# Kernel tuning notes

Hardware: AMD Instinct MI355X
Metric: run time of the kernel (lower is better)

Reference implementation:

```python
import jax, jax.numpy as jnp
import numpy as np

N = 500_000
K = 16
E = N * K
H = 256


def _linear_params(key, fan_in, fan_out):
    k1, k2 = jax.random.split(key)
    bound = 1.0 / np.sqrt(fan_in)
    W = jax.random.uniform(k1, (fan_in, fan_out), jnp.float32, -bound, bound)
    b = jax.random.uniform(k2, (fan_out,), jnp.float32, -bound, bound)
    return W, b


def setup_inputs() -> dict:
    key = jax.random.key(0)
    ks = jax.random.split(key, 10)
    x = jax.random.normal(ks[0], (N, 3), jnp.float32)
    edge_index = jax.random.randint(ks[1], (2, E), 0, N, jnp.int64)
    edge_attr = jax.random.normal(ks[2], (E, 1), jnp.float32)
    W1, b1 = _linear_params(ks[3], K, H)          # GNN1 message MLP: Linear(k, 256)
    We1, be1 = _linear_params(ks[4], H, 128)      # encoder Linear(256,128)
    We2, be2 = _linear_params(ks[5], 128, 6)      # encoder Linear(128,6)
    Wd1, bd1 = _linear_params(ks[6], 6, 128)      # decoder Linear(6,128)
    Wd2, bd2 = _linear_params(ks[7], 128, H)      # decoder Linear(128,256)
    Wo, bo = _linear_params(ks[8], H, 1)          # output Linear(256,1)
    return {"x": x, "edge_index": edge_index, "edge_attr": edge_attr,
            "W1": W1, "b1": b1, "We1": We1, "be1": be1, "We2": We2, "be2": be2,
            "Wd1": Wd1, "bd1": bd1, "Wd2": Wd2, "bd2": bd2, "Wo": Wo, "bo": bo}


def reference(x, edge_index, edge_attr, W1, b1, We1, be1, We2, be2,
              Wd1, bd1, Wd2, bd2, Wo, bo):
    # GNN1: messages are edge_attr verbatim (x_i/x_j ignored); aggregate reshapes
    # all E scalar messages into (N, k) (k edges per node, contiguous) and runs
    # Linear(k,256)+Tanh. Note: LSTM and GCN4 branches in the torch code are dead
    # (GNN1 ignores its node-feature input), so they do not affect the output.
    k = W1.shape[0]
    msgs = edge_attr.reshape(-1, k)                    # (N, k)
    h = jnp.tanh(msgs @ W1 + b1)                       # (N, 256)
    # second L1 call produces the identical result (depends only on edge_attr)
    z = jnp.tanh(jnp.tanh(h @ We1 + be1) @ We2 + be2)  # encoder -> (N, 6)
    d = jnp.tanh(z @ Wd1 + bd1) @ Wd2 + bd2            # decoder -> (N, 256)
    out = jax.nn.sigmoid(jnp.tanh(d) @ Wo + bo)        # (N, 1)
    return out[:, 0]                                   # squeeze(dim=1) -> (N,)
```

## Files before the change

### kernel.cpp

```cpp
#include <hip/hip_runtime.h>


#define N_NODES 500000

#define OFF_W1 0
#define OFF_W2 8192
#define OFF_W3 73728
#define OFF_W4 77824
#define OFF_W5 86016
#define OFF_WO 151552
#define OFF_B1 152576
#define OFF_B2 153600
#define OFF_B3 154112
#define OFF_B4 154176
#define OFF_B5 154688
#define OFF_EXTRA 155712
#define OFF_ZERO  155728
#define IMG_END   156240
#define IMG_ALLOC 156672

#define K1_B1    77824
#define K1_B2    78848
#define K1_B3    79360
#define K1_Z     79872
#define K1_LDS   80384
#define K2_LDS   76800
#define K2_W4    0
#define K2_W5    8192
#define K2_WO    73728
#define K2_B4    74752
#define K2_B5    75264

#define SCONST (-2.8853900817779268f)

typedef _Float16 half8  __attribute__((ext_vector_type(8)));
typedef __fp16   pk16x2 __attribute__((ext_vector_type(2)));
typedef float    f32x4  __attribute__((ext_vector_type(4)));
typedef int      int4v  __attribute__((ext_vector_type(4)));

__device__ __align__(16) char g_img[IMG_ALLOC];

static __device__ __forceinline__ unsigned pack_f16_rne(float a, float b) {
  _Float16 ha = (_Float16)a, hb = (_Float16)b;
  unsigned short ua = __builtin_bit_cast(unsigned short, ha);
  unsigned short ub = __builtin_bit_cast(unsigned short, hb);
  return (unsigned)ua | ((unsigned)ub << 16);
}
static __device__ __forceinline__ int pkrtz(float a, float b) {
  pk16x2 h = __builtin_amdgcn_cvt_pkrtz(a, b);
  return __builtin_bit_cast(int, h);
}
static __device__ __forceinline__ float sig2(float y) {
  float e = __builtin_amdgcn_exp2f(y);
  return __builtin_amdgcn_rcpf(1.0f + e);
}
static __device__ __forceinline__ float sigmoid_f(float x) {
  float e = __builtin_amdgcn_exp2f(x * -1.4426950408889634f);
  return __builtin_amdgcn_rcpf(1.0f + e);
}
static __device__ __forceinline__ f32x4 mfma16(half8 a, int4v b, f32x4 c) {
  return __builtin_amdgcn_mfma_f32_16x16x32_f16(a, __builtin_bit_cast(half8, b), c, 0, 0, 0);
}
static __device__ __forceinline__ half8 lda(const char* smem, int off) {
  return *(const half8*)(smem + off);
}
static __device__ __forceinline__ f32x4 ldf4(const char* smem, int off) {
  return *(const f32x4*)(smem + off);
}
#define FENCE() __builtin_amdgcn_sched_barrier(0)

struct PK2 { int lo, hi; };
static __device__ __forceinline__ PK2 tp(f32x4 a) {
  PK2 p;
  p.lo = pkrtz(sig2(a.x), sig2(a.y));
  p.hi = pkrtz(sig2(a.z), sig2(a.w));
  return p;
}

__global__ void gnn_prep(const float* __restrict__ W1,  const float* __restrict__ b1,
                         const float* __restrict__ We1, const float* __restrict__ be1,
                         const float* __restrict__ We2, const float* __restrict__ be2,
                         const float* __restrict__ Wd1, const float* __restrict__ bd1,
                         const float* __restrict__ Wd2, const float* __restrict__ bd2,
                         const float* __restrict__ Wo,  const float* __restrict__ bo)
{
  int t = blockIdx.x * 256 + threadIdx.x;
  int off = t * 4;
  if (off >= IMG_END) return;
  unsigned val;
  if (off < OFF_W2) {
    int rel = off;
    int mi = rel >> 9, li = (rel >> 4) & 31, j2 = (rel >> 2) & 3;
    int fout = mi * 16 + (li & 15);
    int k0 = (li >> 4) * 8 + j2 * 2;
    val = pack_f16_rne(SCONST * W1[k0 * 256 + fout], SCONST * W1[(k0 + 1) * 256 + fout]);
  } else if (off < OFF_W3) {
    int rel = off - OFF_W2;
    int blk = rel >> 10, li = (rel >> 4) & 63, j2 = (rel >> 2) & 3;
    int mi = blk >> 3, ki = blk & 7;
    int fout = mi * 16 + (li & 15);
    int k0 = ki * 32 + 4 * (li >> 4) + 16 * (j2 >> 1) + 2 * (j2 & 1);
    val = pack_f16_rne(2.0f * SCONST * We1[k0 * 128 + fout],
                       2.0f * SCONST * We1[(k0 + 1) * 128 + fout]);
  } else if (off < OFF_W4) {
    int rel = off - OFF_W3;
    int ki = rel >> 10, li = (rel >> 4) & 63, j2 = (rel >> 2) & 3;
    int fo = li & 15;
    int k0 = ki * 32 + 4 * (li >> 4) + 16 * (j2 >> 1) + 2 * (j2 & 1);
    float a = (fo < 6) ? 2.0f * SCONST * We2[k0 * 6 + fo] : 0.0f;
    float b = (fo < 6) ? 2.0f * SCONST * We2[(k0 + 1) * 6 + fo] : 0.0f;
    val = pack_f16_rne(a, b);
  } else if (off < OFF_W5) {
    int rel = off - OFF_W4;
    int mi = rel >> 10, li = (rel >> 4) & 63, j2 = (rel >> 2) & 3;
    int fout = mi * 16 + (li & 15);
    int qa = li >> 4;
    unsigned v = 0;
    if (j2 < 2) {
      int k0 = 4 * qa + 2 * j2;
      float a = (k0 < 6)     ? 2.0f * SCONST * Wd1[k0 * 128 + fout]       : 0.0f;
      float b = (k0 + 1 < 6) ? 2.0f * SCONST * Wd1[(k0 + 1) * 128 + fout] : 0.0f;
      v = pack_f16_rne(a, b);
    }
    val = v;
  } else if (off < OFF_WO) {
    int rel = off - OFF_W5;
    int blk = rel >> 10, li = (rel >> 4) & 63, j2 = (rel >> 2) & 3;
    int mi = blk >> 2, ki = blk & 3;
    int fout = mi * 16 + (li & 15);
    int k0 = ki * 32 + 4 * (li >> 4) + 16 * (j2 >> 1) + 2 * (j2 & 1);
    val = pack_f16_rne(2.0f * SCONST * Wd2[k0 * 256 + fout],
                       2.0f * SCONST * Wd2[(k0 + 1) * 256 + fout]);
  } else if (off < OFF_B1) {
    val = __builtin_bit_cast(unsigned, 2.0f * Wo[(off - OFF_WO) >> 2]);
  } else if (off < OFF_B2) {
    val = __builtin_bit_cast(unsigned, SCONST * b1[(off - OFF_B1) >> 2]);
  } else if (off < OFF_B3) {
    int i = (off - OFF_B2) >> 2;
    float s = 0.0f;
    for (int k = 0; k < 256; ++k) s += We1[k * 128 + i];
    val = __builtin_bit_cast(unsigned, SCONST * (be1[i] - s));
  } else if (off < OFF_B4) {
    int i = (off - OFF_B3) >> 2;
    float v = 0.0f;
    if (i < 6) {
      float s = 0.0f;
      for (int k = 0; k < 128; ++k) s += We2[k * 6 + i];
      v = SCONST * (be2[i] - s);
    }
    val = __builtin_bit_cast(unsigned, v);
  } else if (off < OFF_B5) {
    int i = (off - OFF_B4) >> 2;
    float s = 0.0f;
    for (int k = 0; k < 6; ++k) s += Wd1[k * 128 + i];
    val = __builtin_bit_cast(unsigned, SCONST * (bd1[i] - s));
  } else if (off < OFF_EXTRA) {
    int i = (off - OFF_B5) >> 2;
    float s = 0.0f;
    for (int k = 0; k < 128; ++k) s += Wd2[k * 256 + i];
    val = __builtin_bit_cast(unsigned, SCONST * (bd2[i] - s));
  } else if (off == OFF_EXTRA) {
    float s = 0.0f;
    for (int k = 0; k < 256; ++k) s += Wo[k];
    val = __builtin_bit_cast(unsigned, bo[0] - s);
  } else {
    val = 0;
  }
  *(unsigned*)(g_img + off) = val;
}

static __device__ __forceinline__ void stage_chunk(const char* src, char* dst) {
  __builtin_amdgcn_global_load_lds(
      (const __attribute__((address_space(1))) void*)src,
      (__attribute__((address_space(3))) void*)dst, 16, 0, 0);
}

#define L1_PAIR(KO, OUT_G0, OUT_G1) do {                                   \
    half8 Ae = lda(smem, w1b + (2*(KO))*w1s);                              \
    half8 Ao = lda(smem, w1b + (2*(KO)+1)*w1s);                            \
    f32x4 be_ = ldf4(smem, K1_B1 + (2*(KO))*64 + q*16);                    \
    f32x4 bo_ = ldf4(smem, K1_B1 + (2*(KO)+1)*64 + q*16);                  \
    f32x4 ae0 = mfma16(Ae, b1g0, be_);                                     \
    f32x4 ae1 = mfma16(Ae, b1g1, be_);                                     \
    f32x4 ao0 = mfma16(Ao, b1g0, bo_);                                     \
    f32x4 ao1 = mfma16(Ao, b1g1, bo_);                                     \
    PK2 pe0 = tp(ae0), po0 = tp(ao0), pe1 = tp(ae1), po1 = tp(ao1);        \
    OUT_G0.x = pe0.lo; OUT_G0.y = pe0.hi; OUT_G0.z = po0.lo; OUT_G0.w = po0.hi; \
    OUT_G1.x = pe1.lo; OUT_G1.y = pe1.hi; OUT_G1.z = po1.lo; OUT_G1.w = po1.hi; \
    FENCE();                                                               \
  } while (0)

#define L2_MI(MI, ACC0, ACC1) do {                                                            \
    f32x4 bb = ldf4(smem, K1_B2 + (MI)*64 + q*16);                                            \
    ACC0 = bb; ACC1 = bb;                                                                     \
    half8 A;                                                                                  \
    A = lda(smem, OFF_W2 + ((MI)*8+0)*1024 + ln*16); ACC0 = mfma16(A, c2g0_0, ACC0); ACC1 = mfma16(A, c2g1_0, ACC1); \
    A = lda(smem, OFF_W2 + ((MI)*8+1)*1024 + ln*16); ACC0 = mfma16(A, c2g0_1, ACC0); ACC1 = mfma16(A, c2g1_1, ACC1); \
    A = lda(smem, OFF_W2 + ((MI)*8+2)*1024 + ln*16); ACC0 = mfma16(A, c2g0_2, ACC0); ACC1 = mfma16(A, c2g1_2, ACC1); \
    A = lda(smem, OFF_W2 + ((MI)*8+3)*1024 + ln*16); ACC0 = mfma16(A, c2g0_3, ACC0); ACC1 = mfma16(A, c2g1_3, ACC1); \
    A = lda(smem, OFF_W2 + ((MI)*8+4)*1024 + ln*16); ACC0 = mfma16(A, c2g0_4, ACC0); ACC1 = mfma16(A, c2g1_4, ACC1); \
    A = lda(smem, OFF_W2 + ((MI)*8+5)*1024 + ln*16); ACC0 = mfma16(A, c2g0_5, ACC0); ACC1 = mfma16(A, c2g1_5, ACC1); \
    A = lda(smem, OFF_W2 + ((MI)*8+6)*1024 + ln*16); ACC0 = mfma16(A, c2g0_6, ACC0); ACC1 = mfma16(A, c2g1_6, ACC1); \
    A = lda(smem, OFF_W2 + ((MI)*8+7)*1024 + ln*16); ACC0 = mfma16(A, c2g0_7, ACC0); ACC1 = mfma16(A, c2g1_7, ACC1); \
  } while (0)

#define L2_PAIR(KO, OUT_G0, OUT_G1) do {                                   \
    f32x4 ve0, ve1, vo0, vo1;                                              \
    L2_MI(2*(KO),   ve0, ve1);                                             \
    FENCE();                                                               \
    L2_MI(2*(KO)+1, vo0, vo1);                                             \
    PK2 pe0 = tp(ve0), po0 = tp(vo0), pe1 = tp(ve1), po1 = tp(vo1);        \
    OUT_G0.x = pe0.lo; OUT_G0.y = pe0.hi; OUT_G0.z = po0.lo; OUT_G0.w = po0.hi; \
    OUT_G1.x = pe1.lo; OUT_G1.y = pe1.hi; OUT_G1.z = po1.lo; OUT_G1.w = po1.hi; \
    FENCE();                                                               \
  } while (0)

__global__ __launch_bounds__(512)
void gnn_k1(const float* __restrict__ ea, int4v* __restrict__ zbuf)
{
  __shared__ __align__(16) char smem[K1_LDS];
  const int tid = threadIdx.x;
  const int wv = tid >> 6, ln = tid & 63;

#pragma unroll 1
  for (int r = 0; r < 10; ++r) {
    int cb = (r * 8 + wv) << 6;
    if (cb < 5024) {
      int src;
      if (cb < 4864)      src = cb * 16;
      else if (cb < 4992) src = OFF_B1 + (cb - 4864) * 16;
      else                src = OFF_ZERO + (cb - 4992) * 16;
      stage_chunk(g_img + src + ln * 16, smem + (size_t)cb * 16 + ln * 16);
    }
  }
  __syncthreads();

  const int q = ln >> 4, c = ln & 15;
  const bool qlo = (q < 2);
  const int lnl16 = (ln & 31) * 16;
  const int w1b = qlo ? (OFF_W1 + lnl16) : (K1_Z + lnl16);
  const int w1s = qlo ? 512 : 0;

  const int NT = (N_NODES + 255) / 256;
#pragma unroll 1
  for (int t = blockIdx.x; t < NT; t += gridDim.x) {
    const int base = t * 256 + wv * 32;

    int nl = base + (q >> 1) * 16 + c;
    if (nl > N_NODES - 1) nl = N_NODES - 1;
    const f32x4* ea4 = (const f32x4*)ea;
    size_t eb = (size_t)nl * 4 + (size_t)((q & 1) * 2);
    f32x4 vlo = ea4[eb];
    f32x4 vhi = ea4[eb + 1];
    int4v b1g0;
    b1g0.x = pkrtz(vlo.x, vlo.y); b1g0.y = pkrtz(vlo.z, vlo.w);
    b1g0.z = pkrtz(vhi.x, vhi.y); b1g0.w = pkrtz(vhi.z, vhi.w);
    int sh = (ln + 32) & 63;
    int4v b1g1;
    b1g1.x = __shfl(b1g0.x, sh, 64); b1g1.y = __shfl(b1g0.y, sh, 64);
    b1g1.z = __shfl(b1g0.z, sh, 64); b1g1.w = __shfl(b1g0.w, sh, 64);

    int4v c2g0_0, c2g0_1, c2g0_2, c2g0_3, c2g0_4, c2g0_5, c2g0_6, c2g0_7;
    int4v c2g1_0, c2g1_1, c2g1_2, c2g1_3, c2g1_4, c2g1_5, c2g1_6, c2g1_7;
    L1_PAIR(0, c2g0_0, c2g1_0);
    L1_PAIR(1, c2g0_1, c2g1_1);
    L1_PAIR(2, c2g0_2, c2g1_2);
    L1_PAIR(3, c2g0_3, c2g1_3);
    L1_PAIR(4, c2g0_4, c2g1_4);
    L1_PAIR(5, c2g0_5, c2g1_5);
    L1_PAIR(6, c2g0_6, c2g1_6);
    L1_PAIR(7, c2g0_7, c2g1_7);

    int4v c3g0_0, c3g0_1, c3g0_2, c3g0_3;
    int4v c3g1_0, c3g1_1, c3g1_2, c3g1_3;
    L2_PAIR(0, c3g0_0, c3g1_0);
    L2_PAIR(1, c3g0_1, c3g1_1);
    L2_PAIR(2, c3g0_2, c3g1_2);
    L2_PAIR(3, c3g0_3, c3g1_3);

    f32x4 bb3 = ldf4(smem, K1_B3 + q * 16);
    f32x4 z0 = bb3, z1 = bb3;
    half8 A;
    A = lda(smem, OFF_W3 + 0 * 1024 + ln * 16); z0 = mfma16(A, c3g0_0, z0); z1 = mfma16(A, c3g1_0, z1);
    A = lda(smem, OFF_W3 + 1 * 1024 + ln * 16); z0 = mfma16(A, c3g0_1, z0); z1 = mfma16(A, c3g1_1, z1);
    A = lda(smem, OFF_W3 + 2 * 1024 + ln * 16); z0 = mfma16(A, c3g0_2, z0); z1 = mfma16(A, c3g1_2, z1);
    A = lda(smem, OFF_W3 + 3 * 1024 + ln * 16); z0 = mfma16(A, c3g0_3, z0); z1 = mfma16(A, c3g1_3, z1);
    PK2 p3g0 = tp(z0);
    PK2 p3g1 = tp(z1);

    if (ln < 32) {
      int4v zv;
      zv.x = p3g0.lo; zv.y = p3g0.hi; zv.z = p3g1.lo; zv.w = p3g1.hi;
      zbuf[(size_t)(t * 8 + wv) * 32 + ln] = zv;
    }
  }
}

#define L4_MI(MI, ACC0, ACC1) do {                                         \
    f32x4 bb = ldf4(smem, K2_B4 + (MI)*64 + q*16);                         \
    half8 A = lda(smem, K2_W4 + (MI)*1024 + ln*16);                        \
    ACC0 = mfma16(A, b4g0, bb);                                            \
    ACC1 = mfma16(A, b4g1, bb);                                            \
  } while (0)

#define L4_PAIR(KO, OUT_G0, OUT_G1) do {                                   \
    f32x4 ve0, ve1, vo0, vo1;                                              \
    L4_MI(2*(KO),   ve0, ve1);                                             \
    L4_MI(2*(KO)+1, vo0, vo1);                                             \
    PK2 pe0 = tp(ve0), po0 = tp(vo0), pe1 = tp(ve1), po1 = tp(vo1);        \
    OUT_G0.x = pe0.lo; OUT_G0.y = pe0.hi; OUT_G0.z = po0.lo; OUT_G0.w = po0.hi; \
    OUT_G1.x = pe1.lo; OUT_G1.y = pe1.hi; OUT_G1.z = po1.lo; OUT_G1.w = po1.hi; \
    FENCE();                                                               \
  } while (0)

#define L5_MI(MI) do {                                                                        \
    f32x4 bb = ldf4(smem, K2_B5 + (MI)*64 + q*16);                                            \
    f32x4 a0 = bb, a1 = bb;                                                                   \
    half8 A;                                                                                  \
    A = lda(smem, K2_W5 + ((MI)*4+0)*1024 + ln*16); a0 = mfma16(A, c5g0_0, a0); a1 = mfma16(A, c5g1_0, a1); \
    A = lda(smem, K2_W5 + ((MI)*4+1)*1024 + ln*16); a0 = mfma16(A, c5g0_1, a0); a1 = mfma16(A, c5g1_1, a1); \
    A = lda(smem, K2_W5 + ((MI)*4+2)*1024 + ln*16); a0 = mfma16(A, c5g0_2, a0); a1 = mfma16(A, c5g1_2, a1); \
    A = lda(smem, K2_W5 + ((MI)*4+3)*1024 + ln*16); a0 = mfma16(A, c5g0_3, a0); a1 = mfma16(A, c5g1_3, a1); \
    f32x4 wo = ldf4(smem, K2_WO + (MI)*64 + q*16);                                            \
    part0 += sig2(a0.x)*wo.x + sig2(a0.y)*wo.y + sig2(a0.z)*wo.z + sig2(a0.w)*wo.w;           \
    part1 += sig2(a1.x)*wo.x + sig2(a1.y)*wo.y + sig2(a1.z)*wo.z + sig2(a1.w)*wo.w;           \
    FENCE();                                                                                  \
  } while (0)

__global__ __launch_bounds__(512)
void gnn_k2(const int4v* __restrict__ zbuf, float* __restrict__ out)
{
  __shared__ __align__(16) char smem[K2_LDS];
  const int tid = threadIdx.x;
  const int wv = tid >> 6, ln = tid & 63;

#pragma unroll 1
  for (int r = 0; r < 10; ++r) {
    int cb = (r * 8 + wv) << 6;
    if (cb < 4800) {
      int src;
      if (cb < 512)       src = OFF_W4 + cb * 16;
      else if (cb < 4672) src = OFF_W5 + (cb - 512) * 16;
      else                src = OFF_B4 + (cb - 4672) * 16;
      stage_chunk(g_img + src + ln * 16, smem + (size_t)cb * 16 + ln * 16);
    }
  }
  __syncthreads();

  const int q = ln >> 4, c = ln & 15;
  const float bo2 = *(const float*)(g_img + OFF_EXTRA);

  const int NT = (N_NODES + 255) / 256;
#pragma unroll 1
  for (int t = blockIdx.x; t < NT; t += gridDim.x) {
    const int base = t * 256 + wv * 32;

    int4v zv = {0, 0, 0, 0};
    if (ln < 32) zv = zbuf[(size_t)(t * 8 + wv) * 32 + ln];

    int4v b4g0, b4g1;
    b4g0.x = zv.x; b4g0.y = zv.y; b4g0.z = 0; b4g0.w = 0;
    b4g1.x = zv.z; b4g1.y = zv.w; b4g1.z = 0; b4g1.w = 0;

    int4v c5g0_0, c5g0_1, c5g0_2, c5g0_3;
    int4v c5g1_0, c5g1_1, c5g1_2, c5g1_3;
    L4_PAIR(0, c5g0_0, c5g1_0);
    L4_PAIR(1, c5g0_1, c5g1_1);
    L4_PAIR(2, c5g0_2, c5g1_2);
    L4_PAIR(3, c5g0_3, c5g1_3);

    float part0 = 0.0f, part1 = 0.0f;
    L5_MI(0);  L5_MI(1);  L5_MI(2);  L5_MI(3);
    L5_MI(4);  L5_MI(5);  L5_MI(6);  L5_MI(7);
    L5_MI(8);  L5_MI(9);  L5_MI(10); L5_MI(11);
    L5_MI(12); L5_MI(13); L5_MI(14); L5_MI(15);

    part0 += __shfl_xor(part0, 16, 64); part0 += __shfl_xor(part0, 32, 64);
    part1 += __shfl_xor(part1, 16, 64); part1 += __shfl_xor(part1, 32, 64);
    if (q < 2) {
      int node = base + q * 16 + c;
      if (node < N_NODES) {
        float v = ((q == 0) ? part0 : part1) + bo2;
        out[node] = sigmoid_f(v);
      }
    }
  }
}

extern "C" void kernel_launch(void* const* d_in, const int* in_sizes, int n_in,
                              void* d_out, int out_size, void* d_ws, size_t ws_size,
                              hipStream_t stream) {
  (void)in_sizes; (void)n_in; (void)ws_size; (void)out_size;
  const float* ea  = (const float*)d_in[2];
  const float* W1  = (const float*)d_in[3];
  const float* b1  = (const float*)d_in[4];
  const float* We1 = (const float*)d_in[5];
  const float* be1 = (const float*)d_in[6];
  const float* We2 = (const float*)d_in[7];
  const float* be2 = (const float*)d_in[8];
  const float* Wd1 = (const float*)d_in[9];
  const float* bd1 = (const float*)d_in[10];
  const float* Wd2 = (const float*)d_in[11];
  const float* bd2 = (const float*)d_in[12];
  const float* Wo  = (const float*)d_in[13];
  const float* bo  = (const float*)d_in[14];

  gnn_prep<<<dim3((IMG_END / 4 + 255) / 256), dim3(256), 0, stream>>>(
      W1, b1, We1, be1, We2, be2, Wd1, bd1, Wd2, bd2, Wo, bo);
  gnn_k1<<<dim3(512), dim3(512), 0, stream>>>(ea, (int4v*)d_ws);
  gnn_k2<<<dim3(512), dim3(512), 0, stream>>>((const int4v*)d_ws, (float*)d_out);
}
```

Baseline: 238.8 us.

## Fuse encoder and decoder kernels into one kernel with full weight image in LDS

Merges the two per-node MLP kernels into a single kernel. The whole packed weight image, about 156KB, is staged into LDS once per block, and each wave processes 32-node groups end to end. This removes the intermediate z buffer write and read through global memory, one kernel launch, and the second weight staging pass. In exchange, blocks grow to 1024 threads with a 128-VGPR cap per thread, so register spills become possible, and only one block fits per CU.

```diff
diff --git a/kernel.cpp b/kernel.cpp
--- a/kernel.cpp
+++ b/kernel.cpp
@@ -19,17 +19,7 @@
 #define IMG_END   156240
 #define IMG_ALLOC 156672
 
-#define K1_B1    77824
-#define K1_B2    78848
-#define K1_B3    79360
-#define K1_Z     79872
-#define K1_LDS   80384
-#define K2_LDS   76800
-#define K2_W4    0
-#define K2_W5    8192
-#define K2_WO    73728
-#define K2_B4    74752
-#define K2_B5    75264
+#define LDS_SZ IMG_ALLOC
 
 #define SCONST (-2.8853900817779268f)
 
@@ -178,8 +168,8 @@
 #define L1_PAIR(KO, OUT_G0, OUT_G1) do {                                   \
     half8 Ae = lda(smem, w1b + (2*(KO))*w1s);                              \
     half8 Ao = lda(smem, w1b + (2*(KO)+1)*w1s);                            \
-    f32x4 be_ = ldf4(smem, K1_B1 + (2*(KO))*64 + q*16);                    \
-    f32x4 bo_ = ldf4(smem, K1_B1 + (2*(KO)+1)*64 + q*16);                  \
+    f32x4 be_ = ldf4(smem, OFF_B1 + (2*(KO))*64 + q*16);                   \
+    f32x4 bo_ = ldf4(smem, OFF_B1 + (2*(KO)+1)*64 + q*16);                 \
     f32x4 ae0 = mfma16(Ae, b1g0, be_);                                     \
     f32x4 ae1 = mfma16(Ae, b1g1, be_);                                     \
     f32x4 ao0 = mfma16(Ao, b1g0, bo_);                                     \
@@ -191,7 +181,7 @@
   } while (0)
 
 #define L2_MI(MI, ACC0, ACC1) do {                                                            \
-    f32x4 bb = ldf4(smem, K1_B2 + (MI)*64 + q*16);                                            \
+    f32x4 bb = ldf4(smem, OFF_B2 + (MI)*64 + q*16);                                           \
     ACC0 = bb; ACC1 = bb;                                                                     \
     half8 A;                                                                                  \
     A = lda(smem, OFF_W2 + ((MI)*8+0)*1024 + ln*16); ACC0 = mfma16(A, c2g0_0, ACC0); ACC1 = mfma16(A, c2g1_0, ACC1); \
@@ -215,22 +205,50 @@
     FENCE();                                                               \
   } while (0)
 
-__global__ __launch_bounds__(512)
-void gnn_k1(const float* __restrict__ ea, int4v* __restrict__ zbuf)
+#define L4_MI(MI, ACC0, ACC1) do {                                         \
+    f32x4 bb = ldf4(smem, OFF_B4 + (MI)*64 + q*16);                        \
+    half8 A = lda(smem, OFF_W4 + (MI)*1024 + ln*16);                       \
+    ACC0 = mfma16(A, b4g0, bb);                                            \
+    ACC1 = mfma16(A, b4g1, bb);                                            \
+  } while (0)
+
+#define L4_PAIR(KO, OUT_G0, OUT_G1) do {                                   \
+    f32x4 ve0, ve1, vo0, vo1;                                              \
+    L4_MI(2*(KO),   ve0, ve1);                                             \
+    L4_MI(2*(KO)+1, vo0, vo1);                                             \
+    PK2 pe0 = tp(ve0), po0 = tp(vo0), pe1 = tp(ve1), po1 = tp(vo1);        \
+    OUT_G0.x = pe0.lo; OUT_G0.y = pe0.hi; OUT_G0.z = po0.lo; OUT_G0.w = po0.hi; \
+    OUT_G1.x = pe1.lo; OUT_G1.y = pe1.hi; OUT_G1.z = po1.lo; OUT_G1.w = po1.hi; \
+    FENCE();                                                               \
+  } while (0)
+
+#define L5_MI(MI) do {                                                                        \
+    f32x4 bb = ldf4(smem, OFF_B5 + (MI)*64 + q*16);                                           \
+    f32x4 a0 = bb, a1 = bb;                                                                   \
+    half8 A;                                                                                  \
+    A = lda(smem, OFF_W5 + ((MI)*4+0)*1024 + ln*16); a0 = mfma16(A, c5g0_0, a0); a1 = mfma16(A, c5g1_0, a1); \
+    A = lda(smem, OFF_W5 + ((MI)*4+1)*1024 + ln*16); a0 = mfma16(A, c5g0_1, a0); a1 = mfma16(A, c5g1_1, a1); \
+    A = lda(smem, OFF_W5 + ((MI)*4+2)*1024 + ln*16); a0 = mfma16(A, c5g0_2, a0); a1 = mfma16(A, c5g1_2, a1); \
+    A = lda(smem, OFF_W5 + ((MI)*4+3)*1024 + ln*16); a0 = mfma16(A, c5g0_3, a0); a1 = mfma16(A, c5g1_3, a1); \
+    f32x4 wo = ldf4(smem, OFF_WO + (MI)*64 + q*16);                                           \
+    part0 += sig2(a0.x)*wo.x + sig2(a0.y)*wo.y + sig2(a0.z)*wo.z + sig2(a0.w)*wo.w;           \
+    part1 += sig2(a1.x)*wo.x + sig2(a1.y)*wo.y + sig2(a1.z)*wo.z + sig2(a1.w)*wo.w;           \
+    FENCE();                                                                                  \
+  } while (0)
+
+__global__ __launch_bounds__(1024)
+void gnn_fused(const float* __restrict__ ea, float* __restrict__ out)
 {
-  __shared__ __align__(16) char smem[K1_LDS];
+  __shared__ __align__(16) char smem[LDS_SZ];
   const int tid = threadIdx.x;
   const int wv = tid >> 6, ln = tid & 63;
 
 #pragma unroll 1
   for (int r = 0; r < 10; ++r) {
-    int cb = (r * 8 + wv) << 6;
-    if (cb < 5024) {
-      int src;
-      if (cb < 4864)      src = cb * 16;
-      else if (cb < 4992) src = OFF_B1 + (cb - 4864) * 16;
-      else                src = OFF_ZERO + (cb - 4992) * 16;
-      stage_chunk(g_img + src + ln * 16, smem + (size_t)cb * 16 + ln * 16);
+    int cb = (r * 16 + wv) << 6;
+    if (cb < 9765) {
+      stage_chunk(g_img + (size_t)cb * 16 + ln * 16,
+                  smem + (size_t)cb * 16 + ln * 16);
     }
   }
   __syncthreads();
@@ -238,13 +256,16 @@
   const int q = ln >> 4, c = ln & 15;
   const bool qlo = (q < 2);
   const int lnl16 = (ln & 31) * 16;
-  const int w1b = qlo ? (OFF_W1 + lnl16) : (K1_Z + lnl16);
+  const int w1b = qlo ? (OFF_W1 + lnl16) : (OFF_ZERO + lnl16);
   const int w1s = qlo ? 512 : 0;
-
-  const int NT = (N_NODES + 255) / 256;
+  const float bo2 = *(const float*)(smem + OFF_EXTRA);
+
+  const int NG = N_NODES / 32;
+  const int g0i = blockIdx.x * 16 + wv;
+  const int gstep = gridDim.x << 4;
 #pragma unroll 1
-  for (int t = blockIdx.x; t < NT; t += gridDim.x) {
-    const int base = t * 256 + wv * 32;
+  for (int g = g0i; g < NG; g += gstep) {
+    const int base = g * 32;
 
     int nl = base + (q >> 1) * 16 + c;
     if (nl > N_NODES - 1) nl = N_NODES - 1;
@@ -278,7 +299,7 @@
     L2_PAIR(2, c3g0_2, c3g1_2);
     L2_PAIR(3, c3g0_3, c3g1_3);
 
-    f32x4 bb3 = ldf4(smem, K1_B3 + q * 16);
+    f32x4 bb3 = ldf4(smem, OFF_B3 + q * 16);
     f32x4 z0 = bb3, z1 = bb3;
     half8 A;
     A = lda(smem, OFF_W3 + 0 * 1024 + ln * 16); z0 = mfma16(A, c3g0_0, z0); z1 = mfma16(A, c3g1_0, z1);
@@ -287,80 +308,11 @@
     A = lda(smem, OFF_W3 + 3 * 1024 + ln * 16); z0 = mfma16(A, c3g0_3, z0); z1 = mfma16(A, c3g1_3, z1);
     PK2 p3g0 = tp(z0);
     PK2 p3g1 = tp(z1);
-
-    if (ln < 32) {
-      int4v zv;
-      zv.x = p3g0.lo; zv.y = p3g0.hi; zv.z = p3g1.lo; zv.w = p3g1.hi;
-      zbuf[(size_t)(t * 8 + wv) * 32 + ln] = zv;
-    }
-  }
-}
-
-#define L4_MI(MI, ACC0, ACC1) do {                                         \
-    f32x4 bb = ldf4(smem, K2_B4 + (MI)*64 + q*16);                         \
-    half8 A = lda(smem, K2_W4 + (MI)*1024 + ln*16);                        \
-    ACC0 = mfma16(A, b4g0, bb);                                            \
-    ACC1 = mfma16(A, b4g1, bb);                                            \
-  } while (0)
-
-#define L4_PAIR(KO, OUT_G0, OUT_G1) do {                                   \
-    f32x4 ve0, ve1, vo0, vo1;                                              \
-    L4_MI(2*(KO),   ve0, ve1);                                             \
-    L4_MI(2*(KO)+1, vo0, vo1);                                             \
-    PK2 pe0 = tp(ve0), po0 = tp(vo0), pe1 = tp(ve1), po1 = tp(vo1);        \
-    OUT_G0.x = pe0.lo; OUT_G0.y = pe0.hi; OUT_G0.z = po0.lo; OUT_G0.w = po0.hi; \
-    OUT_G1.x = pe1.lo; OUT_G1.y = pe1.hi; OUT_G1.z = po1.lo; OUT_G1.w = po1.hi; \
-    FENCE();                                                               \
-  } while (0)
-
-#define L5_MI(MI) do {                                                                        \
-    f32x4 bb = ldf4(smem, K2_B5 + (MI)*64 + q*16);                                            \
-    f32x4 a0 = bb, a1 = bb;                                                                   \
-    half8 A;                                                                                  \
-    A = lda(smem, K2_W5 + ((MI)*4+0)*1024 + ln*16); a0 = mfma16(A, c5g0_0, a0); a1 = mfma16(A, c5g1_0, a1); \
-    A = lda(smem, K2_W5 + ((MI)*4+1)*1024 + ln*16); a0 = mfma16(A, c5g0_1, a0); a1 = mfma16(A, c5g1_1, a1); \
-    A = lda(smem, K2_W5 + ((MI)*4+2)*1024 + ln*16); a0 = mfma16(A, c5g0_2, a0); a1 = mfma16(A, c5g1_2, a1); \
-    A = lda(smem, K2_W5 + ((MI)*4+3)*1024 + ln*16); a0 = mfma16(A, c5g0_3, a0); a1 = mfma16(A, c5g1_3, a1); \
-    f32x4 wo = ldf4(smem, K2_WO + (MI)*64 + q*16);                                            \
-    part0 += sig2(a0.x)*wo.x + sig2(a0.y)*wo.y + sig2(a0.z)*wo.z + sig2(a0.w)*wo.w;           \
-    part1 += sig2(a1.x)*wo.x + sig2(a1.y)*wo.y + sig2(a1.z)*wo.z + sig2(a1.w)*wo.w;           \
-    FENCE();                                                                                  \
-  } while (0)
-
-__global__ __launch_bounds__(512)
-void gnn_k2(const int4v* __restrict__ zbuf, float* __restrict__ out)
-{
-  __shared__ __align__(16) char smem[K2_LDS];
-  const int tid = threadIdx.x;
-  const int wv = tid >> 6, ln = tid & 63;
-
-#pragma unroll 1
-  for (int r = 0; r < 10; ++r) {
-    int cb = (r * 8 + wv) << 6;
-    if (cb < 4800) {
-      int src;
-      if (cb < 512)       src = OFF_W4 + cb * 16;
-      else if (cb < 4672) src = OFF_W5 + (cb - 512) * 16;
-      else                src = OFF_B4 + (cb - 4672) * 16;
-      stage_chunk(g_img + src + ln * 16, smem + (size_t)cb * 16 + ln * 16);
-    }
-  }
-  __syncthreads();
-
-  const int q = ln >> 4, c = ln & 15;
-  const float bo2 = *(const float*)(g_img + OFF_EXTRA);
-
-  const int NT = (N_NODES + 255) / 256;
-#pragma unroll 1
-  for (int t = blockIdx.x; t < NT; t += gridDim.x) {
-    const int base = t * 256 + wv * 32;
-
-    int4v zv = {0, 0, 0, 0};
-    if (ln < 32) zv = zbuf[(size_t)(t * 8 + wv) * 32 + ln];
+    FENCE();
 
     int4v b4g0, b4g1;
-    b4g0.x = zv.x; b4g0.y = zv.y; b4g0.z = 0; b4g0.w = 0;
-    b4g1.x = zv.z; b4g1.y = zv.w; b4g1.z = 0; b4g1.w = 0;
+    b4g0.x = p3g0.lo; b4g0.y = p3g0.hi; b4g0.z = 0; b4g0.w = 0;
+    b4g1.x = p3g1.lo; b4g1.y = p3g1.hi; b4g1.z = 0; b4g1.w = 0;
 
     int4v c5g0_0, c5g0_1, c5g0_2, c5g0_3;
     int4v c5g1_0, c5g1_1, c5g1_2, c5g1_3;
@@ -390,7 +342,7 @@
 extern "C" void kernel_launch(void* const* d_in, const int* in_sizes, int n_in,
                               void* d_out, int out_size, void* d_ws, size_t ws_size,
                               hipStream_t stream) {
-  (void)in_sizes; (void)n_in; (void)ws_size; (void)out_size;
+  (void)in_sizes; (void)n_in; (void)ws_size; (void)out_size; (void)d_ws;
   const float* ea  = (const float*)d_in[2];
   const float* W1  = (const float*)d_in[3];
   const float* b1  = (const float*)d_in[4];
@@ -407,6 +359,5 @@
 
   gnn_prep<<<dim3((IMG_END / 4 + 255) / 256), dim3(256), 0, stream>>>(
       W1, b1, We1, be1, We2, be2, Wd1, bd1, Wd2, bd2, Wo, bo);
-  gnn_k1<<<dim3(512), dim3(512), 0, stream>>>(ea, (int4v*)d_ws);
-  gnn_k2<<<dim3(512), dim3(512), 0, stream>>>((const int4v*)d_ws, (float*)d_out);
-}
+  gnn_fused<<<dim3(256), dim3(1024), 0, stream>>>(ea, (float*)d_out);
+}
```

Result: slower. 289.2 us (+21.1%).
